# Kernel tuning notes

Hardware: AMD Instinct MI355X
Metric: run time of the kernel (lower is better)

Reference implementation:

```python
import jax, jax.numpy as jnp
import numpy as np

N_NODES = 100000
N_EDGES = 1600000
N_GRAPHS = 1000
HID = 64
NEG_SLOPE = 0.2


def _glorot(key, shape):
    fan_in, fan_out = shape[0], shape[-1]
    lim = float(np.sqrt(6.0 / (fan_in + fan_out)))
    return jax.random.uniform(key, shape, jnp.float32, -lim, lim)


def setup_inputs() -> dict:
    key = jax.random.key(0)
    ks = jax.random.split(key, 20)
    x = jax.random.normal(ks[0], (N_NODES, 1), jnp.float32)
    edge_index = jax.random.randint(ks[1], (2, N_EDGES), 0, N_NODES, jnp.int64)
    batch = jnp.sort(jax.random.randint(ks[2], (N_NODES,), 0, N_GRAPHS, jnp.int64))
    inp = {"x": x, "edge_index": edge_index, "batch": batch}
    # GATv2Conv layer 1 (in=3 -> out=HID, 1 head)
    inp["Wl1"] = _glorot(ks[3], (3, HID)); inp["bl1"] = jnp.zeros((HID,), jnp.float32)
    inp["Wr1"] = _glorot(ks[4], (3, HID)); inp["br1"] = jnp.zeros((HID,), jnp.float32)
    inp["a1"] = _glorot(ks[5], (HID, 1))[:, 0]; inp["b1"] = jnp.zeros((HID,), jnp.float32)
    # GATv2Conv layer 2 (HID -> HID)
    inp["Wl2"] = _glorot(ks[6], (HID, HID)); inp["bl2"] = jnp.zeros((HID,), jnp.float32)
    inp["Wr2"] = _glorot(ks[7], (HID, HID)); inp["br2"] = jnp.zeros((HID,), jnp.float32)
    inp["a2"] = _glorot(ks[8], (HID, 1))[:, 0]; inp["b2"] = jnp.zeros((HID,), jnp.float32)
    # lin2 (HID -> 2)
    inp["W3"] = _glorot(ks[9], (HID, 2)); inp["b3"] = jnp.zeros((2,), jnp.float32)
    return inp


def gatv2_layer(x, src, dst, Wl, bl, Wr, br, a, b):
    """GATv2Conv, 1 head, add_self_loops=True, negative_slope=0.2."""
    n = x.shape[0]
    xl = x @ Wl + bl  # source-side transform [N, C]
    xr = x @ Wr + br  # target-side transform [N, C]
    loops = jnp.arange(n, dtype=src.dtype)
    s = jnp.concatenate([src, loops])
    d = jnp.concatenate([dst, loops])
    # per-edge attention logit: a^T LeakyReLU(xl[j] + xr[i])
    e = jax.nn.leaky_relu(xl[s] + xr[d], NEG_SLOPE) @ a  # [E+N]
    # segment softmax over incoming edges of each dst node
    m = jax.ops.segment_max(e, d, num_segments=n)
    ex = jnp.exp(e - m[d])
    denom = jax.ops.segment_sum(ex, d, num_segments=n)
    alpha = ex / denom[d]
    out = jax.ops.segment_sum(alpha[:, None] * xl[s], d, num_segments=n)
    return out + b


def reference(x, edge_index, batch, Wl1, bl1, Wr1, br1, a1, b1,
              Wl2, bl2, Wr2, br2, a2, b2, W3, b3):
    n = x.shape[0]
    src, dst = edge_index[0], edge_index[1]
    ones = jnp.ones((src.shape[0],), jnp.float32)
    deg_in = jax.ops.segment_sum(ones, dst, num_segments=n)   # bincount(dst)
    deg_out = jax.ops.segment_sum(ones, src, num_segments=n)  # bincount(src)
    h = jnp.concatenate([x, deg_in[:, None], deg_out[:, None]], axis=1)  # [N,3]
    h = gatv2_layer(h, src, dst, Wl1, bl1, Wr1, br1, a1, b1)
    h = jnp.tanh(h)
    h = gatv2_layer(h, src, dst, Wl2, bl2, Wr2, br2, a2, b2)
    # global_max_pool over graphs
    g = jax.ops.segment_max(h, batch, num_segments=N_GRAPHS)  # [G, HID]
    return g @ W3 + b3  # [G, 2]
```

## Files before the change

### kernel.cpp

```cpp
#include <hip/hip_runtime.h>
#include <hip/hip_bf16.h>
#include <hip/hip_fp16.h>

#define HID 64
#define NEG_SLOPE 0.2f
#define BLK_E 4096
#define EDGE_CAP 6144
#define NDB 16

typedef _Float16 f16x2 __attribute__((ext_vector_type(2)));


__global__ void k_hist2(const int* __restrict__ src, const int* __restrict__ dst,
                        int* __restrict__ histS, int* __restrict__ histD,
                        int E, int NB, int NBLK) {
    __shared__ int hs[512], hd[512];
    int t = threadIdx.x, blk = blockIdx.x;
    for (int b = t; b < NB; b += 1024) { hs[b] = 0; hd[b] = 0; }
    __syncthreads();
    int base = blk * BLK_E;
    #pragma unroll
    for (int k = 0; k < BLK_E / 1024; ++k) {
        int i = base + k * 1024 + t;
        if (i < E) {
            atomicAdd(&hs[src[i] >> 8], 1);
            atomicAdd(&hd[dst[i] >> 8], 1);
        }
    }
    __syncthreads();
    for (int b = t; b < NB; b += 1024) {
        histS[b * NBLK + blk] = hs[b];
        histD[b * NBLK + blk] = hd[b];
    }
}

__global__ void k_binscan(int* __restrict__ histS, int* __restrict__ histD,
                          int* __restrict__ totS, int* __restrict__ totD,
                          int NB, int NBLK) {
    __shared__ int s[512];
    int b = blockIdx.x;
    int* hist = histS; int* tot = totS;
    if (b >= NB) { b -= NB; hist = histD; tot = totD; }
    int t = threadIdx.x;
    int v = (t < NBLK) ? hist[b * NBLK + t] : 0;
    s[t] = v;
    __syncthreads();
    for (int o = 1; o < 512; o <<= 1) {
        int u = (t >= o) ? s[t - o] : 0;
        __syncthreads();
        s[t] += u;
        __syncthreads();
    }
    if (t < NBLK) hist[b * NBLK + t] = s[t] - v;
    if (t == 511) tot[b] = s[511];
}

__global__ void k_binoffset(const int* __restrict__ totS, const int* __restrict__ totD,
                            int* __restrict__ bsS, int* __restrict__ bsD,
                            int NB, int E, int* __restrict__ row_off, int N) {
    __shared__ int s[512];
    int t = threadIdx.x;
    int v = (t < NB) ? totS[t] : 0;
    s[t] = v; __syncthreads();
    for (int o = 1; o < 512; o <<= 1) {
        int u = (t >= o) ? s[t - o] : 0;
        __syncthreads(); s[t] += u; __syncthreads();
    }
    if (t < NB) bsS[t] = s[t] - v;
    if (t == 0) bsS[NB] = E;
    __syncthreads();
    v = (t < NB) ? totD[t] : 0;
    s[t] = v; __syncthreads();
    for (int o = 1; o < 512; o <<= 1) {
        int u = (t >= o) ? s[t - o] : 0;
        __syncthreads(); s[t] += u; __syncthreads();
    }
    if (t < NB) bsD[t] = s[t] - v;
    if (t == 0) { bsD[NB] = E; row_off[N] = E; }
}

__global__ void k_scatter_bins(const int* __restrict__ src, const int* __restrict__ dst,
                               const int* __restrict__ histS, const int* __restrict__ histD,
                               const int* __restrict__ bsS, const int* __restrict__ bsD,
                               unsigned* __restrict__ packS, unsigned* __restrict__ packD,
                               int E, int NB, int NBLK) {
    __shared__ int baseS[512], baseD[512];
    int t = threadIdx.x, blk = blockIdx.x;
    for (int b = t; b < NB; b += 1024) {
        baseS[b] = bsS[b] + histS[b * NBLK + blk];
        baseD[b] = bsD[b] + histD[b * NBLK + blk];
    }
    __syncthreads();
    int base = blk * BLK_E;
    #pragma unroll
    for (int k = 0; k < BLK_E / 1024; ++k) {
        int i = base + k * 1024 + t;
        if (i < E) {
            int sv = src[i], dv = dst[i];
            int pD = atomicAdd(&baseD[dv >> 8], 1);
            packD[pD] = ((unsigned)(dv & 255) << 24) | (unsigned)sv;
            int pS = atomicAdd(&baseS[sv >> 8], 1);
            packS[pS] = (unsigned)(sv & 255);
        }
    }
}

__global__ void k_csr_bin(const unsigned* __restrict__ packD, const int* __restrict__ bsD,
                          int* __restrict__ row_off, float* __restrict__ deg_in,
                          int* __restrict__ csr_src, int N) {
    __shared__ int cnt[256], off[256], cur[256];
    __shared__ unsigned eb[EDGE_CAP];
    int b = blockIdx.x, t = threadIdx.x;
    int lo = bsD[b], hi = bsD[b + 1], ne = hi - lo;
    bool fits = (ne <= EDGE_CAP);
    if (t < 256) cnt[t] = 0;
    __syncthreads();
    for (int i = t; i < ne; i += 1024) {
        unsigned v = packD[lo + i];
        if (fits) eb[i] = v;
        atomicAdd(&cnt[v >> 24], 1);
    }
    __syncthreads();
    if (t < 256) off[t] = cnt[t];
    __syncthreads();
    for (int o = 1; o < 256; o <<= 1) {
        int u = 0;
        if (t < 256 && t >= o) u = off[t - o];
        __syncthreads();
        if (t < 256) off[t] += u;
        __syncthreads();
    }
    if (t < 256) {
        int ex = off[t] - cnt[t];
        cur[t] = lo + ex;
        int node = b * 256 + t;
        if (node < N) {
            row_off[node] = lo + ex;
            deg_in[node] = (float)cnt[t];
        }
    }
    __syncthreads();
    for (int i = t; i < ne; i += 1024) {
        unsigned v = fits ? eb[i] : packD[lo + i];
        int pos = atomicAdd(&cur[v >> 24], 1);
        csr_src[pos] = (int)(v & 0xFFFFFFu);
    }
}

__global__ void k_cnt_bin(const unsigned* __restrict__ packS, const int* __restrict__ bsS,
                          float* __restrict__ deg_out, int N) {
    __shared__ int cnt[256];
    int b = blockIdx.x, t = threadIdx.x;
    int lo = bsS[b], hi = bsS[b + 1];
    if (t < 256) cnt[t] = 0;
    __syncthreads();
    for (int i = lo + t; i < hi; i += 1024) atomicAdd(&cnt[packS[i] & 255], 1);
    __syncthreads();
    if (t < 256) {
        int node = b * 256 + t;
        if (node < N) deg_out[node] = (float)cnt[t];
    }
}


__global__ void k_deghist(const float* __restrict__ deg_in, int* __restrict__ dhist, int N) {
    __shared__ int h[64];
    int t = threadIdx.x, b = blockIdx.x;
    if (t < 64) h[t] = 0;
    __syncthreads();
    int chunk = (N + NDB - 1) / NDB;
    int lo = b * chunk, hi = lo + chunk; if (hi > N) hi = N;
    for (int i = lo + t; i < hi; i += 1024) {
        int dg = (int)deg_in[i]; if (dg > 63) dg = 63;
        atomicAdd(&h[dg], 1);
    }
    __syncthreads();
    if (t < 64) dhist[t * NDB + b] = h[t];
}

__global__ void k_degscan(int* __restrict__ dhist) {
    __shared__ int s[1024];
    int t = threadIdx.x;
    int v = dhist[t];
    s[t] = v; __syncthreads();
    for (int o = 1; o < 1024; o <<= 1) {
        int u = (t >= o) ? s[t - o] : 0;
        __syncthreads(); s[t] += u; __syncthreads();
    }
    dhist[t] = s[t] - v;
}

__global__ void k_degscatter(const float* __restrict__ deg_in, const int* __restrict__ dhist,
                             int* __restrict__ perm, int N) {
    __shared__ int cur[64];
    int t = threadIdx.x, b = blockIdx.x;
    if (t < 64) cur[t] = dhist[t * NDB + b];
    __syncthreads();
    int chunk = (N + NDB - 1) / NDB;
    int lo = b * chunk, hi = lo + chunk; if (hi > N) hi = N;
    for (int i = lo + t; i < hi; i += 1024) {
        int dg = (int)deg_in[i]; if (dg > 63) dg = 63;
        int p = atomicAdd(&cur[dg], 1);
        perm[p] = i;
    }
}


__global__ void k_xfrm1(const float* __restrict__ x, const float* __restrict__ deg_in,
                        const float* __restrict__ deg_out,
                        const float* __restrict__ Wl, const float* __restrict__ bl,
                        const float* __restrict__ Wr, const float* __restrict__ br,
                        __half* __restrict__ A, __half* __restrict__ B, int N) {
    int idx = blockIdx.x * blockDim.x + threadIdx.x;
    if (idx >= N * HID) return;
    int n = idx >> 6, c = idx & 63;
    float h0 = x[n], h1 = deg_in[n], h2 = deg_out[n];
    A[idx] = __float2half(h0 * Wl[c] + h1 * Wl[HID + c] + h2 * Wl[2 * HID + c] + bl[c]);
    B[idx] = __float2half(h0 * Wr[c] + h1 * Wr[HID + c] + h2 * Wr[2 * HID + c] + br[c]);
}

struct H8 { f16x2 h[8]; };

__device__ __forceinline__ f16x2 bch2(unsigned u) {
    return __builtin_bit_cast(f16x2, u);
}

__device__ __forceinline__ H8 ldrow(const uint4* __restrict__ T, size_t base) {
    uint4 r0 = T[base], r1 = T[base + 1];
    H8 o;
    o.h[0] = bch2(r0.x); o.h[1] = bch2(r0.y); o.h[2] = bch2(r0.z); o.h[3] = bch2(r0.w);
    o.h[4] = bch2(r1.x); o.h[5] = bch2(r1.y); o.h[6] = bch2(r1.z); o.h[7] = bch2(r1.w);
    return o;
}

__device__ __forceinline__ float logit16(const H8& a, const H8& x,
                                         const float* __restrict__ awf, f16x2 ns2) {
    float t = 0.0f;
    #pragma unroll
    for (int j = 0; j < 8; ++j) {
        f16x2 s = a.h[j] + x.h[j];
        f16x2 l = __builtin_elementwise_max(s, ns2 * s);
        t = fmaf((float)l.x, awf[2 * j], t);
        t = fmaf((float)l.y, awf[2 * j + 1], t);
    }
    return t;
}

__device__ __forceinline__ void accum16(float* __restrict__ acc, const H8& a, float w) {
    #pragma unroll
    for (int j = 0; j < 8; ++j) {
        acc[2 * j]     = fmaf((float)a.h[j].x, w, acc[2 * j]);
        acc[2 * j + 1] = fmaf((float)a.h[j].y, w, acc[2 * j + 1]);
    }
}

template <bool TANH>
__global__ void k_gat_fused(const int* __restrict__ csr_src, const int* __restrict__ row_off,
                            const int* __restrict__ perm,
                            const __half* __restrict__ Ah, const __half* __restrict__ Bh,
                            const float* __restrict__ aw, const float* __restrict__ bias,
                            float* __restrict__ out, int N) {
    int tid = blockIdx.x * blockDim.x + threadIdx.x;
    int r = tid >> 2;
    int gl = threadIdx.x & 3;
    if (r >= N) return;
    int d = perm[N - 1 - r];

    const uint4* A16 = (const uint4*)Ah;
    const uint4* B16 = (const uint4*)Bh;
    f16x2 ns2;
    ns2.x = (_Float16)NEG_SLOPE; ns2.y = (_Float16)NEG_SLOPE;

    float awf[16];
    {
        const float4* a4 = (const float4*)aw;
        #pragma unroll
        for (int j = 0; j < 4; ++j) {
            float4 v = a4[gl * 4 + j];
            awf[4 * j] = v.x; awf[4 * j + 1] = v.y; awf[4 * j + 2] = v.z; awf[4 * j + 3] = v.w;
        }
    }

    size_t rowbase = (size_t)d * 8 + gl * 2;
    H8 xh = ldrow(B16, rowbase);
    H8 as = ldrow(A16, rowbase);

    float t = logit16(as, xh, awf, ns2);
    t += __shfl_xor(t, 1); t += __shfl_xor(t, 2);
    float m = t, denom = 1.0f;
    float acc[16];
    #pragma unroll
    for (int j = 0; j < 8; ++j) {
        acc[2 * j] = (float)as.h[j].x;
        acc[2 * j + 1] = (float)as.h[j].y;
    }

    int lo = row_off[d], hi = row_off[d + 1];
    int k = lo;
    for (; k + 3 < hi; k += 4) {
        int s0 = csr_src[k], s1 = csr_src[k + 1], s2 = csr_src[k + 2], s3 = csr_src[k + 3];
        H8 a0 = ldrow(A16, (size_t)s0 * 8 + gl * 2);
        H8 a1 = ldrow(A16, (size_t)s1 * 8 + gl * 2);
        H8 a2 = ldrow(A16, (size_t)s2 * 8 + gl * 2);
        H8 a3 = ldrow(A16, (size_t)s3 * 8 + gl * 2);
        float t0 = logit16(a0, xh, awf, ns2);
        float t1 = logit16(a1, xh, awf, ns2);
        float t2 = logit16(a2, xh, awf, ns2);
        float t3 = logit16(a3, xh, awf, ns2);
        t0 += __shfl_xor(t0, 1); t1 += __shfl_xor(t1, 1);
        t2 += __shfl_xor(t2, 1); t3 += __shfl_xor(t3, 1);
        t0 += __shfl_xor(t0, 2); t1 += __shfl_xor(t1, 2);
        t2 += __shfl_xor(t2, 2); t3 += __shfl_xor(t3, 2);
        float mx = fmaxf(fmaxf(t0, t1), fmaxf(t2, t3));
        if (mx > m) {
            float sc = __expf(m - mx);
            denom *= sc;
            #pragma unroll
            for (int j = 0; j < 16; ++j) acc[j] *= sc;
            m = mx;
        }
        float w0 = __expf(t0 - m), w1 = __expf(t1 - m);
        float w2 = __expf(t2 - m), w3 = __expf(t3 - m);
        denom += (w0 + w1) + (w2 + w3);
        accum16(acc, a0, w0);
        accum16(acc, a1, w1);
        accum16(acc, a2, w2);
        accum16(acc, a3, w3);
    }
    for (; k < hi; ++k) {
        int s0 = csr_src[k];
        H8 a0 = ldrow(A16, (size_t)s0 * 8 + gl * 2);
        float t0 = logit16(a0, xh, awf, ns2);
        t0 += __shfl_xor(t0, 1); t0 += __shfl_xor(t0, 2);
        if (t0 > m) {
            float sc = __expf(m - t0);
            denom *= sc;
            #pragma unroll
            for (int j = 0; j < 16; ++j) acc[j] *= sc;
            m = t0;
        }
        float w0 = __expf(t0 - m);
        denom += w0;
        accum16(acc, a0, w0);
    }

    float inv = 1.0f / denom;
    const float4* b4 = (const float4*)bias;
    float4* o4 = (float4*)out;
    #pragma unroll
    for (int j = 0; j < 4; ++j) {
        float4 bv = b4[gl * 4 + j];
        float4 o;
        o.x = acc[4 * j] * inv + bv.x;
        o.y = acc[4 * j + 1] * inv + bv.y;
        o.z = acc[4 * j + 2] * inv + bv.z;
        o.w = acc[4 * j + 3] * inv + bv.w;
        if (TANH) { o.x = tanhf(o.x); o.y = tanhf(o.y); o.z = tanhf(o.z); o.w = tanhf(o.w); }
        o4[(size_t)d * 16 + gl * 4 + j] = o;
    }
}

__global__ __launch_bounds__(512) void k_xfrm2(
        const float* __restrict__ H,
        const float* __restrict__ Wl, const float* __restrict__ bl,
        const float* __restrict__ Wr, const float* __restrict__ br,
        __half* __restrict__ A, __half* __restrict__ B, int N) {
    __shared__ float wls[4096];
    __shared__ float wrs[4096];
    __shared__ float hst[64 * 66];
    int t = threadIdx.x;
    int base = blockIdx.x * 64;

    ((float4*)wls)[t * 2]     = ((const float4*)Wl)[t * 2];
    ((float4*)wls)[t * 2 + 1] = ((const float4*)Wl)[t * 2 + 1];
    ((float4*)wrs)[t * 2]     = ((const float4*)Wr)[t * 2];
    ((float4*)wrs)[t * 2 + 1] = ((const float4*)Wr)[t * 2 + 1];

    #pragma unroll
    for (int u = 0; u < 2; ++u) {
        int j = t * 2 + u;
        int nd = j >> 4, c4 = j & 15;
        int node = base + nd;
        float4 hv = (node < N) ? ((const float4*)H)[(size_t)node * 16 + c4]
                               : make_float4(0.f, 0.f, 0.f, 0.f);
        hst[(c4 * 4 + 0) * 66 + nd] = hv.x;
        hst[(c4 * 4 + 1) * 66 + nd] = hv.y;
        hst[(c4 * 4 + 2) * 66 + nd] = hv.z;
        hst[(c4 * 4 + 3) * 66 + nd] = hv.w;
    }
    __syncthreads();

    int w = t >> 6, l = t & 63;
    float acL[8] = {0, 0, 0, 0, 0, 0, 0, 0};
    float acR[8] = {0, 0, 0, 0, 0, 0, 0, 0};
    #pragma unroll 4
    for (int kk = 0; kk < 64; ++kk) {
        float hv = hst[kk * 66 + l];
        const float4* wl4 = (const float4*)&wls[kk * 64 + w * 8];
        const float4* wr4 = (const float4*)&wrs[kk * 64 + w * 8];
        float4 w0 = wl4[0], w1 = wl4[1];
        float4 r0 = wr4[0], r1 = wr4[1];
        acL[0] = fmaf(hv, w0.x, acL[0]); acL[1] = fmaf(hv, w0.y, acL[1]);
        acL[2] = fmaf(hv, w0.z, acL[2]); acL[3] = fmaf(hv, w0.w, acL[3]);
        acL[4] = fmaf(hv, w1.x, acL[4]); acL[5] = fmaf(hv, w1.y, acL[5]);
        acL[6] = fmaf(hv, w1.z, acL[6]); acL[7] = fmaf(hv, w1.w, acL[7]);
        acR[0] = fmaf(hv, r0.x, acR[0]); acR[1] = fmaf(hv, r0.y, acR[1]);
        acR[2] = fmaf(hv, r0.z, acR[2]); acR[3] = fmaf(hv, r0.w, acR[3]);
        acR[4] = fmaf(hv, r1.x, acR[4]); acR[5] = fmaf(hv, r1.y, acR[5]);
        acR[6] = fmaf(hv, r1.z, acR[6]); acR[7] = fmaf(hv, r1.w, acR[7]);
    }

    int node = base + l;
    if (node < N) {
        float4 bl0 = ((const float4*)bl)[w * 2], bl1 = ((const float4*)bl)[w * 2 + 1];
        float4 br0 = ((const float4*)br)[w * 2], br1 = ((const float4*)br)[w * 2 + 1];
        __half2* A2 = (__half2*)A;
        __half2* B2 = (__half2*)B;
        size_t bo = (size_t)node * 32 + w * 4;
        A2[bo + 0] = __floats2half2_rn(acL[0] + bl0.x, acL[1] + bl0.y);
        A2[bo + 1] = __floats2half2_rn(acL[2] + bl0.z, acL[3] + bl0.w);
        A2[bo + 2] = __floats2half2_rn(acL[4] + bl1.x, acL[5] + bl1.y);
        A2[bo + 3] = __floats2half2_rn(acL[6] + bl1.z, acL[7] + bl1.w);
        B2[bo + 0] = __floats2half2_rn(acR[0] + br0.x, acR[1] + br0.y);
        B2[bo + 1] = __floats2half2_rn(acR[2] + br0.z, acR[3] + br0.w);
        B2[bo + 2] = __floats2half2_rn(acR[4] + br1.x, acR[5] + br1.y);
        B2[bo + 3] = __floats2half2_rn(acR[6] + br1.z, acR[7] + br1.w);
    }
}

__global__ void k_pool_final(const float* __restrict__ C, const float* __restrict__ b2,
                             const int* __restrict__ batch,
                             const float* __restrict__ W3, const float* __restrict__ b3,
                             float* __restrict__ out, int N, int G) {
    int w = (int)((blockIdx.x * (size_t)blockDim.x + threadIdx.x) >> 6);
    int lane = threadIdx.x & 63;
    if (w >= G) return;
    int lo = 0, hi = N;
    while (lo < hi) { int mid = (lo + hi) >> 1; if (batch[mid] < w) lo = mid + 1; else hi = mid; }
    int s0 = lo;
    hi = N;
    while (lo < hi) { int mid = (lo + hi) >> 1; if (batch[mid] < w + 1) lo = mid + 1; else hi = mid; }
    int e0 = lo;

    float acc = -INFINITY;
    int i = s0;
    for (; i + 3 < e0; i += 4) {
        float v0 = C[(size_t)i * HID + lane];
        float v1 = C[(size_t)(i + 1) * HID + lane];
        float v2 = C[(size_t)(i + 2) * HID + lane];
        float v3 = C[(size_t)(i + 3) * HID + lane];
        acc = fmaxf(acc, fmaxf(fmaxf(v0, v1), fmaxf(v2, v3)));
    }
    for (; i < e0; ++i) acc = fmaxf(acc, C[(size_t)i * HID + lane]);
    float v = acc + b2[lane];

    float p0 = v * W3[lane * 2];
    float p1 = v * W3[lane * 2 + 1];
    #pragma unroll
    for (int o = 32; o; o >>= 1) { p0 += __shfl_xor(p0, o); p1 += __shfl_xor(p1, o); }
    if (lane == 0) {
        out[(size_t)w * 2]     = p0 + b3[0];
        out[(size_t)w * 2 + 1] = p1 + b3[1];
    }
}

extern "C" void kernel_launch(void* const* d_in, const int* in_sizes, int n_in,
                              void* d_out, int out_size, void* d_ws, size_t ws_size,
                              hipStream_t stream) {
    const float* x     = (const float*)d_in[0];
    const int*   ei    = (const int*)d_in[1];
    const int*   batch = (const int*)d_in[2];
    const float* Wl1 = (const float*)d_in[3];
    const float* bl1 = (const float*)d_in[4];
    const float* Wr1 = (const float*)d_in[5];
    const float* br1 = (const float*)d_in[6];
    const float* a1  = (const float*)d_in[7];
    const float* b1  = (const float*)d_in[8];
    const float* Wl2 = (const float*)d_in[9];
    const float* bl2 = (const float*)d_in[10];
    const float* Wr2 = (const float*)d_in[11];
    const float* br2 = (const float*)d_in[12];
    const float* a2  = (const float*)d_in[13];
    const float* b2  = (const float*)d_in[14];
    const float* W3  = (const float*)d_in[15];
    const float* b3  = (const float*)d_in[16];

    const int N = in_sizes[0];
    const int E = in_sizes[1] / 2;
    const int G = out_size / 2;
    const int NB = (N + 255) >> 8;
    const int NBLK = (E + BLK_E - 1) / BLK_E;

    float* ws = (float*)d_ws;
    size_t off = 0;
    float*  C  = ws + off; off += (size_t)N * HID;
    __half* Ah = (__half*)(ws + off); off += (size_t)N * HID / 2;
    __half* Bh = (__half*)(ws + off); off += (size_t)N * HID / 2;
    int*   row_off = (int*)(ws + off); off += N + 1;
    int*   csr_src = (int*)(ws + off); off += E;
    float* deg_in  = ws + off; off += N;
    float* deg_out = ws + off; off += N;
    int*   perm    = (int*)(ws + off); off += N;
    int*   dhist   = (int*)(ws + off); off += 1024;
    int*   bsS  = (int*)(ws + off); off += NB + 1;
    int*   bsD  = (int*)(ws + off); off += NB + 1;
    int*   totS = (int*)(ws + off); off += NB;
    int*   totD = (int*)(ws + off); off += NB;

    unsigned* packD = (unsigned*)C;
    unsigned* packS = packD + E;
    int* histS = (int*)(packS + E);
    int* histD = histS + (size_t)NB * NBLK;

    const int* src  = ei;
    const int* dstp = ei + E;

    const int BT = 256;
    dim3 blk(BT);
    int grid_nodeC = (N * HID + BT - 1) / BT;
    int grid_g4    = (int)(((size_t)N * 4 + BT - 1) / BT);
    int grid_x2    = (N + 63) / 64;

    k_hist2<<<NBLK, 1024, 0, stream>>>(src, dstp, histS, histD, E, NB, NBLK);
    k_binscan<<<2 * NB, 512, 0, stream>>>(histS, histD, totS, totD, NB, NBLK);
    k_binoffset<<<1, 512, 0, stream>>>(totS, totD, bsS, bsD, NB, E, row_off, N);
    k_scatter_bins<<<NBLK, 1024, 0, stream>>>(src, dstp, histS, histD, bsS, bsD,
                                              packS, packD, E, NB, NBLK);
    k_csr_bin<<<NB, 1024, 0, stream>>>(packD, bsD, row_off, deg_in, csr_src, N);
    k_cnt_bin<<<NB, 1024, 0, stream>>>(packS, bsS, deg_out, N);

    k_deghist<<<NDB, 1024, 0, stream>>>(deg_in, dhist, N);
    k_degscan<<<1, 1024, 0, stream>>>(dhist);
    k_degscatter<<<NDB, 1024, 0, stream>>>(deg_in, dhist, perm, N);

    k_xfrm1<<<grid_nodeC, blk, 0, stream>>>(x, deg_in, deg_out, Wl1, bl1, Wr1, br1, Ah, Bh, N);
    k_gat_fused<true><<<grid_g4, blk, 0, stream>>>(csr_src, row_off, perm, Ah, Bh, a1, b1, C, N);

    k_xfrm2<<<grid_x2, 512, 0, stream>>>(C, Wl2, bl2, Wr2, br2, Ah, Bh, N);
    k_gat_fused<false><<<grid_g4, blk, 0, stream>>>(csr_src, row_off, perm, Ah, Bh, a2, b2, C, N);

    k_pool_final<<<(G * 64 + BT - 1) / BT, blk, 0, stream>>>(C, b2, batch, W3, b3,
                                                             (float*)d_out, N, G);
}
```

Baseline: 232.6 us.

## Fuse degree counting and layer-1 transform into CSR build; fp16 intermediate; 8 lanes per node

The out-degree count and the layer-1 feature transform are folded into the CSR binning kernel, which removes two launches and the deg_out round trip. The GAT kernel now uses 8 lanes per destination node instead of 4, with one 16-byte load per lane per neighbor. This raises memory-level parallelism but adds a third shuffle step to each logit reduction. The layer-1 output is stored as fp16 and read by xfrm2 as fp16, halving that traffic at some cost in precision.

```diff
diff --git a/kernel.cpp b/kernel.cpp
--- a/kernel.cpp
+++ b/kernel.cpp
@@ -105,21 +105,28 @@
     }
 }
 
-__global__ void k_csr_bin(const unsigned* __restrict__ packD, const int* __restrict__ bsD,
-                          int* __restrict__ row_off, float* __restrict__ deg_in,
-                          int* __restrict__ csr_src, int N) {
-    __shared__ int cnt[256], off[256], cur[256];
+__global__ void k_csr_bin_fused(const unsigned* __restrict__ packD, const int* __restrict__ bsD,
+                                const unsigned* __restrict__ packS, const int* __restrict__ bsS,
+                                int* __restrict__ row_off, float* __restrict__ deg_in,
+                                int* __restrict__ csr_src,
+                                const float* __restrict__ x,
+                                const float* __restrict__ Wl, const float* __restrict__ bl,
+                                const float* __restrict__ Wr, const float* __restrict__ br,
+                                __half* __restrict__ A, __half* __restrict__ B, int N) {
+    __shared__ int cnt[256], off[256], cur[256], cntS[256];
     __shared__ unsigned eb[EDGE_CAP];
     int b = blockIdx.x, t = threadIdx.x;
     int lo = bsD[b], hi = bsD[b + 1], ne = hi - lo;
     bool fits = (ne <= EDGE_CAP);
-    if (t < 256) cnt[t] = 0;
+    if (t < 256) { cnt[t] = 0; cntS[t] = 0; }
     __syncthreads();
     for (int i = t; i < ne; i += 1024) {
         unsigned v = packD[lo + i];
         if (fits) eb[i] = v;
         atomicAdd(&cnt[v >> 24], 1);
     }
+    int loS = bsS[b], hiS = bsS[b + 1];
+    for (int i = loS + t; i < hiS; i += 1024) atomicAdd(&cntS[packS[i] & 255], 1);
     __syncthreads();
     if (t < 256) off[t] = cnt[t];
     __syncthreads();
@@ -145,20 +152,31 @@
         int pos = atomicAdd(&cur[v >> 24], 1);
         csr_src[pos] = (int)(v & 0xFFFFFFu);
     }
-}
-
-__global__ void k_cnt_bin(const unsigned* __restrict__ packS, const int* __restrict__ bsS,
-                          float* __restrict__ deg_out, int N) {
-    __shared__ int cnt[256];
-    int b = blockIdx.x, t = threadIdx.x;
-    int lo = bsS[b], hi = bsS[b + 1];
-    if (t < 256) cnt[t] = 0;
-    __syncthreads();
-    for (int i = lo + t; i < hi; i += 1024) atomicAdd(&cnt[packS[i] & 255], 1);
-    __syncthreads();
-    if (t < 256) {
-        int node = b * 256 + t;
-        if (node < N) deg_out[node] = (float)cnt[t];
+    int nd = b * 256 + (t >> 2);
+    if (nd < N) {
+        float h0 = x[nd];
+        float h1 = (float)cnt[t >> 2];
+        float h2 = (float)cntS[t >> 2];
+        int c0 = (t & 3) * 16;
+        unsigned ua[4], ub[4];
+        #pragma unroll
+        for (int p = 0; p < 2; ++p) {
+            #pragma unroll
+            for (int q = 0; q < 4; ++q) {
+                int c = c0 + p * 8 + q * 2;
+                float a0 = h0 * Wl[c]     + h1 * Wl[64 + c]     + h2 * Wl[128 + c]     + bl[c];
+                float a1 = h0 * Wl[c + 1] + h1 * Wl[64 + c + 1] + h2 * Wl[128 + c + 1] + bl[c + 1];
+                float b0 = h0 * Wr[c]     + h1 * Wr[64 + c]     + h2 * Wr[128 + c]     + br[c];
+                float b1 = h0 * Wr[c + 1] + h1 * Wr[64 + c + 1] + h2 * Wr[128 + c + 1] + br[c + 1];
+                f16x2 pa; pa.x = (_Float16)a0; pa.y = (_Float16)a1;
+                f16x2 pb; pb.x = (_Float16)b0; pb.y = (_Float16)b1;
+                if (q < 4) { ua[q] = __builtin_bit_cast(unsigned, pa); ub[q] = __builtin_bit_cast(unsigned, pb); }
+            }
+            uint4 sa = make_uint4(ua[0], ua[1], ua[2], ua[3]);
+            uint4 sb = make_uint4(ub[0], ub[1], ub[2], ub[3]);
+            ((uint4*)A)[(size_t)nd * 8 + (t & 3) * 2 + p] = sa;
+            ((uint4*)B)[(size_t)nd * 8 + (t & 3) * 2 + p] = sb;
+        }
     }
 }
 
@@ -206,38 +224,24 @@
 }
 
 
-__global__ void k_xfrm1(const float* __restrict__ x, const float* __restrict__ deg_in,
-                        const float* __restrict__ deg_out,
-                        const float* __restrict__ Wl, const float* __restrict__ bl,
-                        const float* __restrict__ Wr, const float* __restrict__ br,
-                        __half* __restrict__ A, __half* __restrict__ B, int N) {
-    int idx = blockIdx.x * blockDim.x + threadIdx.x;
-    if (idx >= N * HID) return;
-    int n = idx >> 6, c = idx & 63;
-    float h0 = x[n], h1 = deg_in[n], h2 = deg_out[n];
-    A[idx] = __float2half(h0 * Wl[c] + h1 * Wl[HID + c] + h2 * Wl[2 * HID + c] + bl[c]);
-    B[idx] = __float2half(h0 * Wr[c] + h1 * Wr[HID + c] + h2 * Wr[2 * HID + c] + br[c]);
-}
-
-struct H8 { f16x2 h[8]; };
+struct H4 { f16x2 h[4]; };
 
 __device__ __forceinline__ f16x2 bch2(unsigned u) {
     return __builtin_bit_cast(f16x2, u);
 }
 
-__device__ __forceinline__ H8 ldrow(const uint4* __restrict__ T, size_t base) {
-    uint4 r0 = T[base], r1 = T[base + 1];
-    H8 o;
-    o.h[0] = bch2(r0.x); o.h[1] = bch2(r0.y); o.h[2] = bch2(r0.z); o.h[3] = bch2(r0.w);
-    o.h[4] = bch2(r1.x); o.h[5] = bch2(r1.y); o.h[6] = bch2(r1.z); o.h[7] = bch2(r1.w);
+__device__ __forceinline__ H4 ld4(const uint4* __restrict__ T, size_t idx) {
+    uint4 r = T[idx];
+    H4 o;
+    o.h[0] = bch2(r.x); o.h[1] = bch2(r.y); o.h[2] = bch2(r.z); o.h[3] = bch2(r.w);
     return o;
 }
 
-__device__ __forceinline__ float logit16(const H8& a, const H8& x,
-                                         const float* __restrict__ awf, f16x2 ns2) {
+__device__ __forceinline__ float logit8(const H4& a, const H4& x,
+                                        const float* __restrict__ awf, f16x2 ns2) {
     float t = 0.0f;
     #pragma unroll
-    for (int j = 0; j < 8; ++j) {
+    for (int j = 0; j < 4; ++j) {
         f16x2 s = a.h[j] + x.h[j];
         f16x2 l = __builtin_elementwise_max(s, ns2 * s);
         t = fmaf((float)l.x, awf[2 * j], t);
@@ -246,23 +250,23 @@
     return t;
 }
 
-__device__ __forceinline__ void accum16(float* __restrict__ acc, const H8& a, float w) {
-    #pragma unroll
-    for (int j = 0; j < 8; ++j) {
+__device__ __forceinline__ void accum8(float* __restrict__ acc, const H4& a, float w) {
+    #pragma unroll
+    for (int j = 0; j < 4; ++j) {
         acc[2 * j]     = fmaf((float)a.h[j].x, w, acc[2 * j]);
         acc[2 * j + 1] = fmaf((float)a.h[j].y, w, acc[2 * j + 1]);
     }
 }
 
-template <bool TANH>
+template <typename OUT, bool TANH>
 __global__ void k_gat_fused(const int* __restrict__ csr_src, const int* __restrict__ row_off,
                             const int* __restrict__ perm,
                             const __half* __restrict__ Ah, const __half* __restrict__ Bh,
                             const float* __restrict__ aw, const float* __restrict__ bias,
-                            float* __restrict__ out, int N) {
+                            OUT* __restrict__ out, int N) {
     int tid = blockIdx.x * blockDim.x + threadIdx.x;
-    int r = tid >> 2;
-    int gl = threadIdx.x & 3;
+    int r = tid >> 3;
+    int gl = threadIdx.x & 7;
     if (r >= N) return;
     int d = perm[N - 1 - r];
 
@@ -271,26 +275,29 @@
     f16x2 ns2;
     ns2.x = (_Float16)NEG_SLOPE; ns2.y = (_Float16)NEG_SLOPE;
 
-    float awf[16];
+    float awf[8], bw[8];
     {
         const float4* a4 = (const float4*)aw;
+        const float4* b4 = (const float4*)bias;
         #pragma unroll
-        for (int j = 0; j < 4; ++j) {
-            float4 v = a4[gl * 4 + j];
+        for (int j = 0; j < 2; ++j) {
+            float4 v = a4[gl * 2 + j];
             awf[4 * j] = v.x; awf[4 * j + 1] = v.y; awf[4 * j + 2] = v.z; awf[4 * j + 3] = v.w;
-        }
-    }
-
-    size_t rowbase = (size_t)d * 8 + gl * 2;
-    H8 xh = ldrow(B16, rowbase);
-    H8 as = ldrow(A16, rowbase);
-
-    float t = logit16(as, xh, awf, ns2);
-    t += __shfl_xor(t, 1); t += __shfl_xor(t, 2);
+            float4 u = b4[gl * 2 + j];
+            bw[4 * j] = u.x; bw[4 * j + 1] = u.y; bw[4 * j + 2] = u.z; bw[4 * j + 3] = u.w;
+        }
+    }
+
+    size_t rowbase = (size_t)d * 8 + gl;
+    H4 xh = ld4(B16, rowbase);
+    H4 as = ld4(A16, rowbase);
+
+    float t = logit8(as, xh, awf, ns2);
+    t += __shfl_xor(t, 1); t += __shfl_xor(t, 2); t += __shfl_xor(t, 4);
     float m = t, denom = 1.0f;
-    float acc[16];
-    #pragma unroll
-    for (int j = 0; j < 8; ++j) {
+    float acc[8];
+    #pragma unroll
+    for (int j = 0; j < 4; ++j) {
         acc[2 * j] = (float)as.h[j].x;
         acc[2 * j + 1] = (float)as.h[j].y;
     }
@@ -299,69 +306,77 @@
     int k = lo;
     for (; k + 3 < hi; k += 4) {
         int s0 = csr_src[k], s1 = csr_src[k + 1], s2 = csr_src[k + 2], s3 = csr_src[k + 3];
-        H8 a0 = ldrow(A16, (size_t)s0 * 8 + gl * 2);
-        H8 a1 = ldrow(A16, (size_t)s1 * 8 + gl * 2);
-        H8 a2 = ldrow(A16, (size_t)s2 * 8 + gl * 2);
-        H8 a3 = ldrow(A16, (size_t)s3 * 8 + gl * 2);
-        float t0 = logit16(a0, xh, awf, ns2);
-        float t1 = logit16(a1, xh, awf, ns2);
-        float t2 = logit16(a2, xh, awf, ns2);
-        float t3 = logit16(a3, xh, awf, ns2);
+        H4 a0 = ld4(A16, (size_t)s0 * 8 + gl);
+        H4 a1 = ld4(A16, (size_t)s1 * 8 + gl);
+        H4 a2 = ld4(A16, (size_t)s2 * 8 + gl);
+        H4 a3 = ld4(A16, (size_t)s3 * 8 + gl);
+        float t0 = logit8(a0, xh, awf, ns2);
+        float t1 = logit8(a1, xh, awf, ns2);
+        float t2 = logit8(a2, xh, awf, ns2);
+        float t3 = logit8(a3, xh, awf, ns2);
         t0 += __shfl_xor(t0, 1); t1 += __shfl_xor(t1, 1);
         t2 += __shfl_xor(t2, 1); t3 += __shfl_xor(t3, 1);
         t0 += __shfl_xor(t0, 2); t1 += __shfl_xor(t1, 2);
         t2 += __shfl_xor(t2, 2); t3 += __shfl_xor(t3, 2);
+        t0 += __shfl_xor(t0, 4); t1 += __shfl_xor(t1, 4);
+        t2 += __shfl_xor(t2, 4); t3 += __shfl_xor(t3, 4);
         float mx = fmaxf(fmaxf(t0, t1), fmaxf(t2, t3));
         if (mx > m) {
             float sc = __expf(m - mx);
             denom *= sc;
             #pragma unroll
-            for (int j = 0; j < 16; ++j) acc[j] *= sc;
+            for (int j = 0; j < 8; ++j) acc[j] *= sc;
             m = mx;
         }
         float w0 = __expf(t0 - m), w1 = __expf(t1 - m);
         float w2 = __expf(t2 - m), w3 = __expf(t3 - m);
         denom += (w0 + w1) + (w2 + w3);
-        accum16(acc, a0, w0);
-        accum16(acc, a1, w1);
-        accum16(acc, a2, w2);
-        accum16(acc, a3, w3);
+        accum8(acc, a0, w0);
+        accum8(acc, a1, w1);
+        accum8(acc, a2, w2);
+        accum8(acc, a3, w3);
     }
     for (; k < hi; ++k) {
         int s0 = csr_src[k];
-        H8 a0 = ldrow(A16, (size_t)s0 * 8 + gl * 2);
-        float t0 = logit16(a0, xh, awf, ns2);
-        t0 += __shfl_xor(t0, 1); t0 += __shfl_xor(t0, 2);
+        H4 a0 = ld4(A16, (size_t)s0 * 8 + gl);
+        float t0 = logit8(a0, xh, awf, ns2);
+        t0 += __shfl_xor(t0, 1); t0 += __shfl_xor(t0, 2); t0 += __shfl_xor(t0, 4);
         if (t0 > m) {
             float sc = __expf(m - t0);
             denom *= sc;
             #pragma unroll
-            for (int j = 0; j < 16; ++j) acc[j] *= sc;
+            for (int j = 0; j < 8; ++j) acc[j] *= sc;
             m = t0;
         }
         float w0 = __expf(t0 - m);
         denom += w0;
-        accum16(acc, a0, w0);
+        accum8(acc, a0, w0);
     }
 
     float inv = 1.0f / denom;
-    const float4* b4 = (const float4*)bias;
-    float4* o4 = (float4*)out;
-    #pragma unroll
-    for (int j = 0; j < 4; ++j) {
-        float4 bv = b4[gl * 4 + j];
-        float4 o;
-        o.x = acc[4 * j] * inv + bv.x;
-        o.y = acc[4 * j + 1] * inv + bv.y;
-        o.z = acc[4 * j + 2] * inv + bv.z;
-        o.w = acc[4 * j + 3] * inv + bv.w;
-        if (TANH) { o.x = tanhf(o.x); o.y = tanhf(o.y); o.z = tanhf(o.z); o.w = tanhf(o.w); }
-        o4[(size_t)d * 16 + gl * 4 + j] = o;
+    float v[8];
+    #pragma unroll
+    for (int j = 0; j < 8; ++j) {
+        v[j] = acc[j] * inv + bw[j];
+        if (TANH) v[j] = tanhf(v[j]);
+    }
+    if constexpr (sizeof(OUT) == 2) {
+        unsigned u[4];
+        #pragma unroll
+        for (int j = 0; j < 4; ++j) {
+            f16x2 p; p.x = (_Float16)v[2 * j]; p.y = (_Float16)v[2 * j + 1];
+            u[j] = __builtin_bit_cast(unsigned, p);
+        }
+        ((uint4*)out)[(size_t)d * 8 + gl] = make_uint4(u[0], u[1], u[2], u[3]);
+    } else {
+        float4* o4 = (float4*)out;
+        o4[(size_t)d * 16 + gl * 2]     = make_float4(v[0], v[1], v[2], v[3]);
+        o4[(size_t)d * 16 + gl * 2 + 1] = make_float4(v[4], v[5], v[6], v[7]);
     }
 }
 
 __global__ __launch_bounds__(512) void k_xfrm2(
-        const float* __restrict__ H,
+        const __half* __restrict__ H,
         const float* __restrict__ Wl, const float* __restrict__ bl,
         const float* __restrict__ Wr, const float* __restrict__ br,
         __half* __restrict__ A, __half* __restrict__ B, int N) {
@@ -376,17 +391,21 @@
     ((float4*)wrs)[t * 2]     = ((const float4*)Wr)[t * 2];
     ((float4*)wrs)[t * 2 + 1] = ((const float4*)Wr)[t * 2 + 1];
 
-    #pragma unroll
-    for (int u = 0; u < 2; ++u) {
-        int j = t * 2 + u;
-        int nd = j >> 4, c4 = j & 15;
+    {
+        int nd = t >> 3, q = t & 7;
         int node = base + nd;
-        float4 hv = (node < N) ? ((const float4*)H)[(size_t)node * 16 + c4]
-                               : make_float4(0.f, 0.f, 0.f, 0.f);
-        hst[(c4 * 4 + 0) * 66 + nd] = hv.x;
-        hst[(c4 * 4 + 1) * 66 + nd] = hv.y;
-        hst[(c4 * 4 + 2) * 66 + nd] = hv.z;
-        hst[(c4 * 4 + 3) * 66 + nd] = hv.w;
+        uint4 hv = (node < N) ? ((const uint4*)H)[(size_t)node * 8 + q]
+                              : make_uint4(0, 0, 0, 0);
+        f16x2 p0 = bch2(hv.x), p1 = bch2(hv.y), p2 = bch2(hv.z), p3 = bch2(hv.w);
+        int c = q * 8;
+        hst[(c + 0) * 66 + nd] = (float)p0.x;
+        hst[(c + 1) * 66 + nd] = (float)p0.y;
+        hst[(c + 2) * 66 + nd] = (float)p1.x;
+        hst[(c + 3) * 66 + nd] = (float)p1.y;
+        hst[(c + 4) * 66 + nd] = (float)p2.x;
+        hst[(c + 5) * 66 + nd] = (float)p2.y;
+        hst[(c + 6) * 66 + nd] = (float)p3.x;
+        hst[(c + 7) * 66 + nd] = (float)p3.y;
     }
     __syncthreads();
 
@@ -499,7 +518,6 @@
     int*   row_off = (int*)(ws + off); off += N + 1;
     int*   csr_src = (int*)(ws + off); off += E;
     float* deg_in  = ws + off; off += N;
-    float* deg_out = ws + off; off += N;
     int*   perm    = (int*)(ws + off); off += N;
     int*   dhist   = (int*)(ws + off); off += 1024;
     int*   bsS  = (int*)(ws + off); off += NB + 1;
@@ -511,33 +529,34 @@
     unsigned* packS = packD + E;
     int* histS = (int*)(packS + E);
     int* histD = histS + (size_t)NB * NBLK;
+    __half* Chalf = (__half*)C;
 
     const int* src  = ei;
     const int* dstp = ei + E;
 
     const int BT = 256;
     dim3 blk(BT);
-    int grid_nodeC = (N * HID + BT - 1) / BT;
-    int grid_g4    = (int)(((size_t)N * 4 + BT - 1) / BT);
-    int grid_x2    = (N + 63) / 64;
+    int grid_g8 = (int)(((size_t)N * 8 + BT - 1) / BT);
+    int grid_x2 = (N + 63) / 64;
 
     k_hist2<<<NBLK, 1024, 0, stream>>>(src, dstp, histS, histD, E, NB, NBLK);
     k_binscan<<<2 * NB, 512, 0, stream>>>(histS, histD, totS, totD, NB, NBLK);
     k_binoffset<<<1, 512, 0, stream>>>(totS, totD, bsS, bsD, NB, E, row_off, N);
     k_scatter_bins<<<NBLK, 1024, 0, stream>>>(src, dstp, histS, histD, bsS, bsD,
                                               packS, packD, E, NB, NBLK);
-    k_csr_bin<<<NB, 1024, 0, stream>>>(packD, bsD, row_off, deg_in, csr_src, N);
-    k_cnt_bin<<<NB, 1024, 0, stream>>>(packS, bsS, deg_out, N);
+    k_csr_bin_fused<<<NB, 1024, 0, stream>>>(packD, bsD, packS, bsS, row_off, deg_in,
+                                             csr_src, x, Wl1, bl1, Wr1, br1, Ah, Bh, N);
 
     k_deghist<<<NDB, 1024, 0, stream>>>(deg_in, dhist, N);
     k_degscan<<<1, 1024, 0, stream>>>(dhist);
     k_degscatter<<<NDB, 1024, 0, stream>>>(deg_in, dhist, perm, N);
 
-    k_xfrm1<<<grid_nodeC, blk, 0, stream>>>(x, deg_in, deg_out, Wl1, bl1, Wr1, br1, Ah, Bh, N);
-    k_gat_fused<true><<<grid_g4, blk, 0, stream>>>(csr_src, row_off, perm, Ah, Bh, a1, b1, C, N);
-
-    k_xfrm2<<<grid_x2, 512, 0, stream>>>(C, Wl2, bl2, Wr2, br2, Ah, Bh, N);
-    k_gat_fused<false><<<grid_g4, blk, 0, stream>>>(csr_src, row_off, perm, Ah, Bh, a2, b2, C, N);
+    k_gat_fused<__half, true><<<grid_g8, blk, 0, stream>>>(csr_src, row_off, perm,
+                                                           Ah, Bh, a1, b1, Chalf, N);
+
+    k_xfrm2<<<grid_x2, 512, 0, stream>>>(Chalf, Wl2, bl2, Wr2, br2, Ah, Bh, N);
+    k_gat_fused<float, false><<<grid_g8, blk, 0, stream>>>(csr_src, row_off, perm,
+                                                           Ah, Bh, a2, b2, C, N);
 
     k_pool_final<<<(G * 64 + BT - 1) / BT, blk, 0, stream>>>(C, b2, batch, W3, b3,
                                                              (float*)d_out, N, G);
```

Result: faster. 218.1 us (-6.2%).
